# Kernel tuning notes

Hardware: AMD Instinct MI355X
Metric: run time of the kernel (lower is better)

The kernel has to match this reference:

```python
import jax, jax.numpy as jnp
import numpy as np
from jax import lax

B, T, F, H = 64, 512, 512, 1024
NUM_LAYERS = 2


def setup_inputs() -> dict:
    key = jax.random.key(0)
    ks = jax.random.split(key, 9)
    s = 0.05  # small init scale to keep gates in a sane range
    inp = {
        "x": jax.random.normal(ks[0], (B, T, F), dtype=jnp.float32),
        "W_ih_0": jax.random.normal(ks[1], (4 * H, F), dtype=jnp.float32) * s,
        "W_hh_0": jax.random.normal(ks[2], (4 * H, H), dtype=jnp.float32) * s,
        "b_ih_0": jax.random.normal(ks[3], (4 * H,), dtype=jnp.float32) * s,
        "b_hh_0": jax.random.normal(ks[4], (4 * H,), dtype=jnp.float32) * s,
        "W_ih_1": jax.random.normal(ks[5], (4 * H, H), dtype=jnp.float32) * s,
        "W_hh_1": jax.random.normal(ks[6], (4 * H, H), dtype=jnp.float32) * s,
        "b_ih_1": jax.random.normal(ks[7], (4 * H,), dtype=jnp.float32) * s,
        "b_hh_1": jax.random.normal(ks[8], (4 * H,), dtype=jnp.float32) * s,
    }
    return inp


def _lstm_cell(xin, h, c, Wi, Wh, bi, bh):
    # PyTorch LSTMCell: gates ordered (i, f, g, o)
    gates = xin @ Wi.T + h @ Wh.T + bi + bh  # [B, 4H]
    i, f, g, o = jnp.split(gates, 4, axis=-1)
    c_new = jax.nn.sigmoid(f) * c + jax.nn.sigmoid(i) * jnp.tanh(g)
    h_new = jax.nn.sigmoid(o) * jnp.tanh(c_new)
    return h_new, c_new


def reference(x, W_ih_0, W_hh_0, b_ih_0, b_hh_0, W_ih_1, W_hh_1, b_ih_1, b_hh_1):
    params = [(W_ih_0, W_hh_0, b_ih_0, b_hh_0), (W_ih_1, W_hh_1, b_ih_1, b_hh_1)]
    bsz = x.shape[0]

    def step(carry, xt):
        hs, cs = carry
        new_h, new_c = [], []
        inp = xt
        for (Wi, Wh, bi, bh), h, c in zip(params, hs, cs):
            h, c = _lstm_cell(inp, h, c, Wi, Wh, bi, bh)
            new_h.append(h)
            new_c.append(c)
            inp = h
        return (tuple(new_h), tuple(new_c)), inp  # top-layer h is the output

    zeros = tuple(jnp.zeros((bsz, H), dtype=x.dtype) for _ in range(NUM_LAYERS))
    (hT, cT), ys = lax.scan(step, (zeros, zeros), jnp.swapaxes(x, 0, 1))  # ys: [T, B, H]
    out = jnp.swapaxes(ys, 0, 1)  # [B, T, H], sequence_channel=1
    # final state: ([num_layers, B, H], [num_layers, B, H]) as in return_full_states=False
    return out, jnp.stack(hT, 0), jnp.stack(cT, 0)
```

## Files before the change

kernel.cpp:

```cpp
#include <hip/hip_runtime.h>

#define TSTEPS 512
#define BATCH  64
#define FEAT   512
#define HID    1024
#define NWG    256
#define NTHR   256

typedef _Float16 half8_t  __attribute__((ext_vector_type(8)));
typedef _Float16 half4_t  __attribute__((ext_vector_type(4)));
typedef float    float4_t __attribute__((ext_vector_type(4)));

__device__ __forceinline__ float sigf(float x)      { return 1.0f / (1.0f + __expf(-x)); }
__device__ __forceinline__ float tanh_fast(float x) { return 2.0f / (1.0f + __expf(-2.0f * x)) - 1.0f; }

__global__ void xpose_kernel(const float* __restrict__ x, _Float16* __restrict__ xT) {
    int idx = blockIdx.x * NTHR + threadIdx.x;
    int f4 = idx & 127;
    int bt = idx >> 7;
    int t = bt & (TSTEPS - 1);
    int b = bt >> 9;
    float4_t v = ((const float4_t*)x)[idx];
    half4_t h;
    h.x = (_Float16)v.x; h.y = (_Float16)v.y; h.z = (_Float16)v.z; h.w = (_Float16)v.w;
    *(half4_t*)(xT + (size_t)(t * BATCH + b) * FEAT + f4 * 4) = h;
}

__device__ __forceinline__ void grid_barrier(unsigned* bar, int line_id, unsigned step) {
    __syncthreads();
    if (threadIdx.x == 0) {
        unsigned* gen  = bar;
        unsigned* root = bar + 32;
        unsigned* line = bar + 64 + 32 * line_id;
        unsigned old = __hip_atomic_fetch_add(line, 1u, __ATOMIC_RELEASE, __HIP_MEMORY_SCOPE_AGENT);
        if (old == 32u * step - 1u) {
            unsigned r = __hip_atomic_fetch_add(root, 1u, __ATOMIC_RELEASE, __HIP_MEMORY_SCOPE_AGENT);
            if (r == 8u * step - 1u)
                __hip_atomic_store(gen, step, __ATOMIC_RELEASE, __HIP_MEMORY_SCOPE_AGENT);
        }
        while (__hip_atomic_load(gen, __ATOMIC_RELAXED, __HIP_MEMORY_SCOPE_AGENT) < step)
            __builtin_amdgcn_s_sleep(1);
    }
    __syncthreads();
    __builtin_amdgcn_fence(__ATOMIC_ACQUIRE, "agent");
}

__global__ __launch_bounds__(NTHR, 1) void lstm_persistent(
    const float* __restrict__ Wih0, const float* __restrict__ Whh0,
    const float* __restrict__ bih0, const float* __restrict__ bhh0,
    const float* __restrict__ Wih1, const float* __restrict__ Whh1,
    const float* __restrict__ bih1, const float* __restrict__ bhh1,
    const _Float16* __restrict__ xT,
    _Float16* __restrict__ h0buf,
    _Float16* __restrict__ h1buf,
    unsigned* __restrict__ bar,
    float* __restrict__ out)
{
    extern __shared__ __align__(16) char smem[];
    _Float16* w0x = (_Float16*)smem;
    _Float16* w0h = w0x + 16 * FEAT;
    _Float16* w1  = w0h + 16 * HID;

    const int wg  = blockIdx.x;
    const int u0  = ((wg & 7) * 32 + (wg >> 3)) * 4;
    const int tid = threadIdx.x;

    for (int idx = tid; idx < 16 * FEAT; idx += NTHR) {
        int m = idx >> 9, k = idx & (FEAT - 1);
        int grow = (m & 3) * HID + u0 + (m >> 2);
        w0x[(((k >> 3) * 16) + m) * 8 + (k & 7)] = (_Float16)Wih0[grow * FEAT + k];
    }
    for (int idx = tid; idx < 16 * HID; idx += NTHR) {
        int m = idx >> 10, k = idx & (HID - 1);
        int grow = (m & 3) * HID + u0 + (m >> 2);
        w0h[(((k >> 3) * 16) + m) * 8 + (k & 7)] = (_Float16)Whh0[grow * HID + k];
    }
    for (int idx = tid; idx < 16 * 2048; idx += NTHR) {
        int m = idx >> 11, k = idx & 2047;
        int grow = (m & 3) * HID + u0 + (m >> 2);
        float v = (k < HID) ? Wih1[grow * HID + k] : Whh1[grow * HID + (k - HID)];
        w1[(((k >> 3) * 16) + m) * 8 + (k & 7)] = (_Float16)v;
    }

    const int lane  = tid & 63;
    const int wv    = tid >> 6;
    const int q     = lane >> 4;
    const int n     = lane & 15;
    const int batch = wv * 16 + n;
    const int unit  = u0 + q;

    float b0r[4], b1r[4];
#pragma unroll
    for (int r = 0; r < 4; ++r) {
        int grow = r * HID + unit;
        b0r[r] = bih0[grow] + bhh0[grow];
        b1r[r] = bih1[grow] + bhh1[grow];
    }

    __syncthreads();

    const half8_t* a0x = (const half8_t*)w0x;
    const half8_t* a0h = (const half8_t*)w0h;
    const half8_t* a1  = (const half8_t*)w1;
    const float4_t fzero = {0.f, 0.f, 0.f, 0.f};

    float c0 = 0.f, c1 = 0.f, h0v = 0.f, h1v = 0.f;
    float4_t acc[4];
    half8_t  xreg[16];

    {
        const _Float16* xb = xT + (size_t)batch * FEAT + q * 8;
        acc[0] = fzero; acc[1] = fzero; acc[2] = fzero; acc[3] = fzero;
#pragma unroll
        for (int s = 0; s < 16; ++s)
            acc[s & 3] = __builtin_amdgcn_mfma_f32_16x16x32_f16(
                a0x[(s * 4 + q) * 16 + n], *(const half8_t*)(xb + s * 32), acc[s & 3], 0, 0, 0);
        float4_t g = (acc[0] + acc[1]) + (acc[2] + acc[3]);
        float I = sigf(g.x + b0r[0]);
        float G = tanh_fast(g.z + b0r[2]);
        float O = sigf(g.w + b0r[3]);
        c0  = I * G;
        h0v = O * tanh_fast(c0);
        h0buf[batch * HID + unit] = (_Float16)h0v;
    }
    {
        const _Float16* xb = xT + ((size_t)BATCH + batch) * FEAT + q * 8;
#pragma unroll
        for (int s = 0; s < 16; ++s) xreg[s] = *(const half8_t*)(xb + s * 32);
    }
    grid_barrier(bar, wg & 7, 1u);

    for (int t = 0; t < TSTEPS; ++t) {
        const _Float16* h0cur = h0buf + (t & 1) * (BATCH * HID) + batch * HID + q * 8;
        half8_t p0r[32];
#pragma unroll
        for (int s = 0; s < 32; ++s) p0r[s] = *(const half8_t*)(h0cur + s * 32);

        acc[0] = fzero; acc[1] = fzero; acc[2] = fzero; acc[3] = fzero;
#pragma unroll 8
        for (int s = 0; s < 32; ++s)
            acc[s & 3] = __builtin_amdgcn_mfma_f32_16x16x32_f16(
                a1[(s * 4 + q) * 16 + n], p0r[s], acc[s & 3], 0, 0, 0);
        {
            const _Float16* p1 = h1buf + ((t & 1) ^ 1) * (BATCH * HID) + batch * HID + q * 8;
#pragma unroll 8
            for (int s = 0; s < 32; ++s)
                acc[s & 3] = __builtin_amdgcn_mfma_f32_16x16x32_f16(
                    a1[(128 + s * 4 + q) * 16 + n], *(const half8_t*)(p1 + s * 32), acc[s & 3], 0, 0, 0);
        }
        {
            float4_t g = (acc[0] + acc[1]) + (acc[2] + acc[3]);
            float I = sigf(g.x + b1r[0]);
            float F = sigf(g.y + b1r[1]);
            float G = tanh_fast(g.z + b1r[2]);
            float O = sigf(g.w + b1r[3]);
            c1  = F * c1 + I * G;
            h1v = O * tanh_fast(c1);
        }
        h1buf[(t & 1) * (BATCH * HID) + batch * HID + unit] = (_Float16)h1v;
        out[((size_t)batch * TSTEPS + t) * HID + unit] = h1v;

        if (t + 1 < TSTEPS) {
            if (t + 2 < TSTEPS) {
                const _Float16* xb = xT + ((size_t)(t + 2) * BATCH + batch) * FEAT + q * 8;
#pragma unroll
                for (int s = 0; s < 16; ++s) xreg[s] = *(const half8_t*)(xb + s * 32);
            }
            acc[0] = fzero; acc[1] = fzero; acc[2] = fzero; acc[3] = fzero;
#pragma unroll 8
            for (int s = 0; s < 16; ++s)
                acc[s & 3] = __builtin_amdgcn_mfma_f32_16x16x32_f16(
                    a0x[(s * 4 + q) * 16 + n], xreg[s], acc[s & 3], 0, 0, 0);
#pragma unroll 8
            for (int s = 0; s < 32; ++s)
                acc[s & 3] = __builtin_amdgcn_mfma_f32_16x16x32_f16(
                    a0h[(s * 4 + q) * 16 + n], p0r[s], acc[s & 3], 0, 0, 0);
            {
                float4_t g = (acc[0] + acc[1]) + (acc[2] + acc[3]);
                float I = sigf(g.x + b0r[0]);
                float F = sigf(g.y + b0r[1]);
                float G = tanh_fast(g.z + b0r[2]);
                float O = sigf(g.w + b0r[3]);
                c0  = F * c0 + I * G;
                h0v = O * tanh_fast(c0);
            }
            h0buf[((t + 1) & 1) * (BATCH * HID) + batch * HID + unit] = (_Float16)h0v;
            grid_barrier(bar, wg & 7, (unsigned)(t + 2));
        }
    }

    float* hT = out + (size_t)BATCH * TSTEPS * HID;
    float* cT = hT + 2 * BATCH * HID;
    hT[batch * HID + unit]               = h0v;
    hT[BATCH * HID + batch * HID + unit] = h1v;
    cT[batch * HID + unit]               = c0;
    cT[BATCH * HID + batch * HID + unit] = c1;
}

__global__ __launch_bounds__(NTHR, 1) void lstm_persistent2(
    const float* __restrict__ Wih0, const float* __restrict__ Whh0,
    const float* __restrict__ bih0, const float* __restrict__ bhh0,
    const float* __restrict__ Wih1, const float* __restrict__ Whh1,
    const float* __restrict__ bih1, const float* __restrict__ bhh1,
    const _Float16* __restrict__ xT,
    _Float16* __restrict__ h0buf, _Float16* __restrict__ h1buf,
    unsigned* __restrict__ bar, float* __restrict__ out)
{
    extern __shared__ __align__(16) char smem[];
    _Float16* w0x = (_Float16*)smem;
    _Float16* w0h = w0x + 16 * FEAT;
    _Float16* w1  = w0h + 16 * HID;

    const int wg  = blockIdx.x;
    const int u0  = ((wg & 7) * 32 + (wg >> 3)) * 4;
    const int tid = threadIdx.x;

    for (int idx = tid; idx < 16 * FEAT; idx += NTHR) {
        int m = idx >> 9, k = idx & (FEAT - 1);
        int grow = (m & 3) * HID + u0 + (m >> 2);
        w0x[(((k >> 3) * 16) + m) * 8 + (k & 7)] = (_Float16)Wih0[grow * FEAT + k];
    }
    for (int idx = tid; idx < 16 * HID; idx += NTHR) {
        int m = idx >> 10, k = idx & (HID - 1);
        int grow = (m & 3) * HID + u0 + (m >> 2);
        w0h[(((k >> 3) * 16) + m) * 8 + (k & 7)] = (_Float16)Whh0[grow * HID + k];
    }
    for (int idx = tid; idx < 16 * 2048; idx += NTHR) {
        int m = idx >> 11, k = idx & 2047;
        int grow = (m & 3) * HID + u0 + (m >> 2);
        float v = (k < HID) ? Wih1[grow * HID + k] : Whh1[grow * HID + (k - HID)];
        w1[(((k >> 3) * 16) + m) * 8 + (k & 7)] = (_Float16)v;
    }

    const int lane  = tid & 63;
    const int wv    = tid >> 6;
    const int q     = lane >> 4;
    const int n     = lane & 15;
    const int batch = wv * 16 + n;
    const int unit  = u0 + q;

    float b0r[4], b1r[4];
#pragma unroll
    for (int r = 0; r < 4; ++r) {
        int grow = r * HID + unit;
        b0r[r] = bih0[grow] + bhh0[grow];
        b1r[r] = bih1[grow] + bhh1[grow];
    }

    __syncthreads();

    const half8_t* a0x = (const half8_t*)w0x;
    const half8_t* a0h = (const half8_t*)w0h;
    const half8_t* a1  = (const half8_t*)w1;
    const float4_t fzero = {0.f, 0.f, 0.f, 0.f};

    float c0 = 0.f, c1 = 0.f, h0v = 0.f, h1v = 0.f;
    float4_t acc[4];
    half8_t  xreg[16];

    {
        const _Float16* xb = xT + (size_t)batch * FEAT + q * 8;
        acc[0] = fzero; acc[1] = fzero; acc[2] = fzero; acc[3] = fzero;
#pragma unroll
        for (int s = 0; s < 16; ++s)
            acc[s & 3] = __builtin_amdgcn_mfma_f32_16x16x32_f16(
                a0x[(s * 4 + q) * 16 + n], *(const half8_t*)(xb + s * 32), acc[s & 3], 0, 0, 0);
        float4_t g = (acc[0] + acc[1]) + (acc[2] + acc[3]);
        float I = sigf(g.x + b0r[0]);
        float G = tanh_fast(g.z + b0r[2]);
        float O = sigf(g.w + b0r[3]);
        c0  = I * G;
        h0v = O * tanh_fast(c0);
        h0buf[batch * HID + unit] = (_Float16)h0v;
    }
    {
        const _Float16* xb = xT + ((size_t)BATCH + batch) * FEAT + q * 8;
#pragma unroll
        for (int s = 0; s < 16; ++s) xreg[s] = *(const half8_t*)(xb + s * 32);
    }
    grid_barrier(bar, wg & 7, 1u);

    for (int t = 0; t < TSTEPS; ++t) {
        const _Float16* h0cur = h0buf + (t & 1) * (BATCH * HID) + batch * HID + q * 8;
        half8_t p0r[32];
#pragma unroll
        for (int s = 0; s < 32; ++s) p0r[s] = *(const half8_t*)(h0cur + s * 32);

        acc[0] = fzero; acc[1] = fzero; acc[2] = fzero; acc[3] = fzero;
#pragma unroll 8
        for (int s = 0; s < 32; ++s)
            acc[s & 3] = __builtin_amdgcn_mfma_f32_16x16x32_f16(
                a1[(s * 4 + q) * 16 + n], p0r[s], acc[s & 3], 0, 0, 0);
        {
            const _Float16* p1 = h1buf + ((t & 1) ^ 1) * (BATCH * HID) + batch * HID + q * 8;
#pragma unroll 8
            for (int s = 0; s < 32; ++s)
                acc[s & 3] = __builtin_amdgcn_mfma_f32_16x16x32_f16(
                    a1[(128 + s * 4 + q) * 16 + n], *(const half8_t*)(p1 + s * 32), acc[s & 3], 0, 0, 0);
        }
        {
            float4_t g = (acc[0] + acc[1]) + (acc[2] + acc[3]);
            float I = sigf(g.x + b1r[0]);
            float F = sigf(g.y + b1r[1]);
            float G = tanh_fast(g.z + b1r[2]);
            float O = sigf(g.w + b1r[3]);
            c1  = F * c1 + I * G;
            h1v = O * tanh_fast(c1);
        }
        h1buf[(t & 1) * (BATCH * HID) + batch * HID + unit] = (_Float16)h1v;
        out[((size_t)batch * TSTEPS + t) * HID + unit] = h1v;

        if (t + 1 < TSTEPS) {
            acc[0] = fzero; acc[1] = fzero; acc[2] = fzero; acc[3] = fzero;
#pragma unroll 8
            for (int s = 0; s < 16; ++s)
                acc[s & 3] = __builtin_amdgcn_mfma_f32_16x16x32_f16(
                    a0x[(s * 4 + q) * 16 + n], xreg[s], acc[s & 3], 0, 0, 0);
#pragma unroll 8
            for (int s = 0; s < 32; ++s)
                acc[s & 3] = __builtin_amdgcn_mfma_f32_16x16x32_f16(
                    a0h[(s * 4 + q) * 16 + n], p0r[s], acc[s & 3], 0, 0, 0);
            {
                float4_t g = (acc[0] + acc[1]) + (acc[2] + acc[3]);
                float I = sigf(g.x + b0r[0]);
                float F = sigf(g.y + b0r[1]);
                float G = tanh_fast(g.z + b0r[2]);
                float O = sigf(g.w + b0r[3]);
                c0  = F * c0 + I * G;
                h0v = O * tanh_fast(c0);
            }
            h0buf[((t + 1) & 1) * (BATCH * HID) + batch * HID + unit] = (_Float16)h0v;
            if (t + 2 < TSTEPS) {
                const _Float16* xb = xT + ((size_t)(t + 2) * BATCH + batch) * FEAT + q * 8;
#pragma unroll
                for (int s = 0; s < 16; ++s) xreg[s] = *(const half8_t*)(xb + s * 32);
            }
            grid_barrier(bar, wg & 7, (unsigned)(t + 2));
        }
    }

    float* hT = out + (size_t)BATCH * TSTEPS * HID;
    float* cT = hT + 2 * BATCH * HID;
    hT[batch * HID + unit]               = h0v;
    hT[BATCH * HID + batch * HID + unit] = h1v;
    cT[batch * HID + unit]               = c0;
    cT[BATCH * HID + batch * HID + unit] = c1;
}

extern "C" void kernel_launch(void* const* d_in, const int* in_sizes, int n_in,
                              void* d_out, int out_size, void* d_ws, size_t ws_size,
                              hipStream_t stream) {
    (void)in_sizes; (void)n_in; (void)out_size; (void)ws_size;
    const float* x    = (const float*)d_in[0];
    const float* Wih0 = (const float*)d_in[1];
    const float* Whh0 = (const float*)d_in[2];
    const float* bih0 = (const float*)d_in[3];
    const float* bhh0 = (const float*)d_in[4];
    const float* Wih1 = (const float*)d_in[5];
    const float* Whh1 = (const float*)d_in[6];
    const float* bih1 = (const float*)d_in[7];
    const float* bhh1 = (const float*)d_in[8];

    char* ws = (char*)d_ws;
    unsigned* bar   = (unsigned*)ws;
    _Float16* h0buf = (_Float16*)(ws + 4096);
    _Float16* h1buf = (_Float16*)(ws + 4096 + 2 * BATCH * HID * sizeof(_Float16));
    _Float16* xT    = (_Float16*)(ws + (1 << 20));

    hipMemsetAsync(d_ws, 0, 1 << 20, stream);

    xpose_kernel<<<(BATCH * TSTEPS * FEAT / 4) / NTHR, NTHR, 0, stream>>>(x, xT);

    const int shmem = 16 * (FEAT + HID + 2048) * (int)sizeof(_Float16);
    hipFuncSetAttribute((const void*)lstm_persistent2,
                        hipFuncAttributeMaxDynamicSharedMemorySize, shmem);
    lstm_persistent2<<<NWG, NTHR, shmem, stream>>>(
        Wih0, Whh0, bih0, bhh0, Wih1, Whh1, bih1, bhh1,
        xT, h0buf, h1buf, bar, (float*)d_out);
}
```

Measured before the change: 22.06 ms.

## Stage hidden states per XCD with crew copy and drop transpose kernel

Each workgroup detects its XCD, and the workgroups on an XCD cooperatively copy the global h0/h1 state and the fp16-converted next x slice into a per-XCD staging buffer after each grid barrier. A second per-XCD barrier then lets compute read from the XCD-local copy, so it hits that XCD's L2 instead of cross-XCD lines. The separate x transpose kernel is removed and the x conversion is folded into the crew copy. This adds an extra barrier and a copy phase on the critical path of every timestep.

Result: slower. 26.75 ms (+21.2%).

```diff
diff --git a/kernel.cpp b/kernel.cpp
--- a/kernel.cpp
+++ b/kernel.cpp
@@ -6,25 +6,17 @@
 #define HID    1024
 #define NWG    256
 #define NTHR   256
-
+#define WPL    (BATCH * HID / 4)
+#define STGULL 40960
+#define AGENT  __HIP_MEMORY_SCOPE_AGENT
+
+typedef unsigned long long ull;
 typedef _Float16 half8_t  __attribute__((ext_vector_type(8)));
 typedef _Float16 half4_t  __attribute__((ext_vector_type(4)));
 typedef float    float4_t __attribute__((ext_vector_type(4)));
 
 __device__ __forceinline__ float sigf(float x)      { return 1.0f / (1.0f + __expf(-x)); }
 __device__ __forceinline__ float tanh_fast(float x) { return 2.0f / (1.0f + __expf(-2.0f * x)) - 1.0f; }
-
-__global__ void xpose_kernel(const float* __restrict__ x, _Float16* __restrict__ xT) {
-    int idx = blockIdx.x * NTHR + threadIdx.x;
-    int f4 = idx & 127;
-    int bt = idx >> 7;
-    int t = bt & (TSTEPS - 1);
-    int b = bt >> 9;
-    float4_t v = ((const float4_t*)x)[idx];
-    half4_t h;
-    h.x = (_Float16)v.x; h.y = (_Float16)v.y; h.z = (_Float16)v.z; h.w = (_Float16)v.w;
-    *(half4_t*)(xT + (size_t)(t * BATCH + b) * FEAT + f4 * 4) = h;
-}
 
 __device__ __forceinline__ void grid_barrier(unsigned* bar, int line_id, unsigned step) {
     __syncthreads();
@@ -32,27 +24,74 @@
         unsigned* gen  = bar;
         unsigned* root = bar + 32;
         unsigned* line = bar + 64 + 32 * line_id;
-        unsigned old = __hip_atomic_fetch_add(line, 1u, __ATOMIC_RELEASE, __HIP_MEMORY_SCOPE_AGENT);
+        unsigned old = __hip_atomic_fetch_add(line, 1u, __ATOMIC_RELEASE, AGENT);
         if (old == 32u * step - 1u) {
-            unsigned r = __hip_atomic_fetch_add(root, 1u, __ATOMIC_RELEASE, __HIP_MEMORY_SCOPE_AGENT);
+            unsigned r = __hip_atomic_fetch_add(root, 1u, __ATOMIC_RELEASE, AGENT);
             if (r == 8u * step - 1u)
-                __hip_atomic_store(gen, step, __ATOMIC_RELEASE, __HIP_MEMORY_SCOPE_AGENT);
-        }
-        while (__hip_atomic_load(gen, __ATOMIC_RELAXED, __HIP_MEMORY_SCOPE_AGENT) < step)
+                __hip_atomic_store(gen, step, __ATOMIC_RELEASE, AGENT);
+        }
+        while (__hip_atomic_load(gen, __ATOMIC_RELAXED, AGENT) < step)
             __builtin_amdgcn_s_sleep(1);
     }
     __syncthreads();
     __builtin_amdgcn_fence(__ATOMIC_ACQUIRE, "agent");
 }
 
-__global__ __launch_bounds__(NTHR, 1) void lstm_persistent(
+__device__ __forceinline__ void xbar_sync(unsigned* xb, int tid, unsigned target) {
+    __syncthreads();
+    if (tid == 0) {
+        __hip_atomic_fetch_add(xb, 1u, __ATOMIC_RELEASE, AGENT);
+        while (__hip_atomic_load(xb, __ATOMIC_RELAXED, AGENT) < target)
+            __builtin_amdgcn_s_sleep(1);
+    }
+    __syncthreads();
+    asm volatile("" ::: "memory");
+    __builtin_amdgcn_sched_barrier(0);
+}
+
+__device__ __forceinline__ void crew_copy(ull* stg, const ull* h0src, const ull* h1src,
+                                          const float* x, int t2, int do_x,
+                                          int slot, int tid, int crewN) {
+    if (crewN == 32) {
+        int idx = slot * NTHR + tid;
+        ull a = h0src[idx];
+        ull b = h0src[idx + 8192];
+        ull c = h1src[idx];
+        ull d = h1src[idx + 8192];
+        stg[idx]         = a;  stg[idx + 8192]         = b;
+        stg[16384 + idx] = c;  stg[16384 + idx + 8192] = d;
+        if (do_x) {
+            int bb = idx >> 7, f4 = idx & 127;
+            float4_t v = *(const float4_t*)(x + ((size_t)bb * TSTEPS + t2) * FEAT + f4 * 4);
+            half4_t h;
+            h.x = (_Float16)v.x; h.y = (_Float16)v.y; h.z = (_Float16)v.z; h.w = (_Float16)v.w;
+            ((half4_t*)(stg + 32768))[idx] = h;
+        }
+    } else {
+        for (int w = slot * NTHR + tid; w < 16384; w += crewN * NTHR) {
+            stg[w]         = h0src[w];
+            stg[16384 + w] = h1src[w];
+        }
+        if (do_x)
+            for (int idx = slot * NTHR + tid; idx < 8192; idx += crewN * NTHR) {
+                int bb = idx >> 7, f4 = idx & 127;
+                float4_t v = *(const float4_t*)(x + ((size_t)bb * TSTEPS + t2) * FEAT + f4 * 4);
+                half4_t h;
+                h.x = (_Float16)v.x; h.y = (_Float16)v.y; h.z = (_Float16)v.z; h.w = (_Float16)v.w;
+                ((half4_t*)(stg + 32768))[idx] = h;
+            }
+    }
+}
+
+__global__ __launch_bounds__(NTHR, 1) void lstm_persistent4(
     const float* __restrict__ Wih0, const float* __restrict__ Whh0,
     const float* __restrict__ bih0, const float* __restrict__ bhh0,
     const float* __restrict__ Wih1, const float* __restrict__ Whh1,
     const float* __restrict__ bih1, const float* __restrict__ bhh1,
-    const _Float16* __restrict__ xT,
-    _Float16* __restrict__ h0buf,
-    _Float16* __restrict__ h1buf,
+    const float* __restrict__ xf,
+    ull* __restrict__ hx0,
+    ull* __restrict__ hx1,
+    ull* __restrict__ stage,
     unsigned* __restrict__ bar,
     float* __restrict__ out)
 {
@@ -60,10 +99,21 @@
     _Float16* w0x = (_Float16*)smem;
     _Float16* w0h = w0x + 16 * FEAT;
     _Float16* w1  = w0h + 16 * HID;
+    int* comm = (int*)(w1 + 16 * 2048);
 
     const int wg  = blockIdx.x;
     const int u0  = ((wg & 7) * 32 + (wg >> 3)) * 4;
     const int tid = threadIdx.x;
+
+    unsigned* crewcnt = bar + 512;
+    unsigned* xbars   = bar + 1024;
+
+    if (tid == 0) {
+        unsigned xcc = __builtin_amdgcn_s_getreg(63508) & 15u;
+        unsigned slot = __hip_atomic_fetch_add(crewcnt + 32 * xcc, 1u, __ATOMIC_RELAXED, AGENT);
+        comm[0] = (int)xcc;
+        comm[1] = (int)slot;
+    }
 
     for (int idx = tid; idx < 16 * FEAT; idx += NTHR) {
         int m = idx >> 9, k = idx & (FEAT - 1);
@@ -99,6 +149,18 @@
 
     __syncthreads();
 
+    const int xcd  = comm[0];
+    const int slot = comm[1];
+    unsigned* xbar = xbars + 32 * xcd;
+    ull* stg       = stage + (size_t)xcd * STGULL;
+    const _Float16* sh   = (const _Float16*)stg;
+    const _Float16* myh0 = sh + batch * HID + q * 8;
+    const _Float16* myh1 = sh + BATCH * HID + batch * HID + q * 8;
+    const _Float16* myx  = sh + 2 * BATCH * HID + batch * FEAT + q * 8;
+
+    _Float16* hx0h = (_Float16*)hx0;
+    _Float16* hx1h = (_Float16*)hx1;
+
     const half8_t* a0x = (const half8_t*)w0x;
     const half8_t* a0h = (const half8_t*)w0h;
     const half8_t* a1  = (const half8_t*)w1;
@@ -106,48 +168,52 @@
 
     float c0 = 0.f, c1 = 0.f, h0v = 0.f, h1v = 0.f;
     float4_t acc[4];
-    half8_t  xreg[16];
 
     {
-        const _Float16* xb = xT + (size_t)batch * FEAT + q * 8;
+        const float* xb = xf + (size_t)batch * (TSTEPS * FEAT) + q * 8;
         acc[0] = fzero; acc[1] = fzero; acc[2] = fzero; acc[3] = fzero;
 #pragma unroll
-        for (int s = 0; s < 16; ++s)
+        for (int s = 0; s < 16; ++s) {
+            float4_t v0 = *(const float4_t*)(xb + s * 32);
+            float4_t v1 = *(const float4_t*)(xb + s * 32 + 4);
+            half8_t xfr;
+            xfr[0] = (_Float16)v0.x; xfr[1] = (_Float16)v0.y;
+            xfr[2] = (_Float16)v0.z; xfr[3] = (_Float16)v0.w;
+            xfr[4] = (_Float16)v1.x; xfr[5] = (_Float16)v1.y;
+            xfr[6] = (_Float16)v1.z; xfr[7] = (_Float16)v1.w;
             acc[s & 3] = __builtin_amdgcn_mfma_f32_16x16x32_f16(
-                a0x[(s * 4 + q) * 16 + n], *(const half8_t*)(xb + s * 32), acc[s & 3], 0, 0, 0);
+                a0x[(s * 4 + q) * 16 + n], xfr, acc[s & 3], 0, 0, 0);
+        }
         float4_t g = (acc[0] + acc[1]) + (acc[2] + acc[3]);
         float I = sigf(g.x + b0r[0]);
         float G = tanh_fast(g.z + b0r[2]);
         float O = sigf(g.w + b0r[3]);
         c0  = I * G;
         h0v = O * tanh_fast(c0);
-        h0buf[batch * HID + unit] = (_Float16)h0v;
-    }
-    {
-        const _Float16* xb = xT + ((size_t)BATCH + batch) * FEAT + q * 8;
-#pragma unroll
-        for (int s = 0; s < 16; ++s) xreg[s] = *(const half8_t*)(xb + s * 32);
+        hx0h[batch * HID + unit] = (_Float16)h0v;
     }
     grid_barrier(bar, wg & 7, 1u);
+    if (tid == 0)
+        comm[2] = (int)__hip_atomic_load(crewcnt + 32 * xcd, __ATOMIC_RELAXED, AGENT);
+    __syncthreads();
+    const int crewN = comm[2];
+    crew_copy(stg, hx0, hx1 + WPL, xf, 1, 1, slot, tid, crewN);
+    xbar_sync(xbar, tid, (unsigned)crewN);
 
     for (int t = 0; t < TSTEPS; ++t) {
-        const _Float16* h0cur = h0buf + (t & 1) * (BATCH * HID) + batch * HID + q * 8;
         half8_t p0r[32];
 #pragma unroll
-        for (int s = 0; s < 32; ++s) p0r[s] = *(const half8_t*)(h0cur + s * 32);
+        for (int s = 0; s < 32; ++s) p0r[s] = *(const half8_t*)(myh0 + s * 32);
 
         acc[0] = fzero; acc[1] = fzero; acc[2] = fzero; acc[3] = fzero;
 #pragma unroll 8
         for (int s = 0; s < 32; ++s)
             acc[s & 3] = __builtin_amdgcn_mfma_f32_16x16x32_f16(
                 a1[(s * 4 + q) * 16 + n], p0r[s], acc[s & 3], 0, 0, 0);
-        {
-            const _Float16* p1 = h1buf + ((t & 1) ^ 1) * (BATCH * HID) + batch * HID + q * 8;
-#pragma unroll 8
-            for (int s = 0; s < 32; ++s)
-                acc[s & 3] = __builtin_amdgcn_mfma_f32_16x16x32_f16(
-                    a1[(128 + s * 4 + q) * 16 + n], *(const half8_t*)(p1 + s * 32), acc[s & 3], 0, 0, 0);
-        }
+#pragma unroll 8
+        for (int s = 0; s < 32; ++s)
+            acc[s & 3] = __builtin_amdgcn_mfma_f32_16x16x32_f16(
+                a1[(128 + s * 4 + q) * 16 + n], *(const half8_t*)(myh1 + s * 32), acc[s & 3], 0, 0, 0);
         {
             float4_t g = (acc[0] + acc[1]) + (acc[2] + acc[3]);
             float I = sigf(g.x + b1r[0]);
@@ -157,20 +223,16 @@
             c1  = F * c1 + I * G;
             h1v = O * tanh_fast(c1);
         }
-        h1buf[(t & 1) * (BATCH * HID) + batch * HID + unit] = (_Float16)h1v;
         out[((size_t)batch * TSTEPS + t) * HID + unit] = h1v;
 
         if (t + 1 < TSTEPS) {
-            if (t + 2 < TSTEPS) {
-                const _Float16* xb = xT + ((size_t)(t + 2) * BATCH + batch) * FEAT + q * 8;
-#pragma unroll
-                for (int s = 0; s < 16; ++s) xreg[s] = *(const half8_t*)(xb + s * 32);
-            }
+            hx1h[(t & 1) * (BATCH * HID) + batch * HID + unit] = (_Float16)h1v;
+
             acc[0] = fzero; acc[1] = fzero; acc[2] = fzero; acc[3] = fzero;
 #pragma unroll 8
             for (int s = 0; s < 16; ++s)
                 acc[s & 3] = __builtin_amdgcn_mfma_f32_16x16x32_f16(
-                    a0x[(s * 4 + q) * 16 + n], xreg[s], acc[s & 3], 0, 0, 0);
+                    a0x[(s * 4 + q) * 16 + n], *(const half8_t*)(myx + s * 32), acc[s & 3], 0, 0, 0);
 #pragma unroll 8
             for (int s = 0; s < 32; ++s)
                 acc[s & 3] = __builtin_amdgcn_mfma_f32_16x16x32_f16(
@@ -184,158 +246,15 @@
                 c0  = F * c0 + I * G;
                 h0v = O * tanh_fast(c0);
             }
-            h0buf[((t + 1) & 1) * (BATCH * HID) + batch * HID + unit] = (_Float16)h0v;
+            hx0h[((t + 1) & 1) * (BATCH * HID) + batch * HID + unit] = (_Float16)h0v;
+
             grid_barrier(bar, wg & 7, (unsigned)(t + 2));
-        }
-    }
-
-    float* hT = out + (size_t)BATCH * TSTEPS * HID;
-    float* cT = hT + 2 * BATCH * HID;
-    hT[batch * HID + unit]               = h0v;
-    hT[BATCH * HID + batch * HID + unit] = h1v;
-    cT[batch * HID + unit]               = c0;
-    cT[BATCH * HID + batch * HID + unit] = c1;
-}
-
-__global__ __launch_bounds__(NTHR, 1) void lstm_persistent2(
-    const float* __restrict__ Wih0, const float* __restrict__ Whh0,
-    const float* __restrict__ bih0, const float* __restrict__ bhh0,
-    const float* __restrict__ Wih1, const float* __restrict__ Whh1,
-    const float* __restrict__ bih1, const float* __restrict__ bhh1,
-    const _Float16* __restrict__ xT,
-    _Float16* __restrict__ h0buf, _Float16* __restrict__ h1buf,
-    unsigned* __restrict__ bar, float* __restrict__ out)
-{
-    extern __shared__ __align__(16) char smem[];
-    _Float16* w0x = (_Float16*)smem;
-    _Float16* w0h = w0x + 16 * FEAT;
-    _Float16* w1  = w0h + 16 * HID;
-
-    const int wg  = blockIdx.x;
-    const int u0  = ((wg & 7) * 32 + (wg >> 3)) * 4;
-    const int tid = threadIdx.x;
-
-    for (int idx = tid; idx < 16 * FEAT; idx += NTHR) {
-        int m = idx >> 9, k = idx & (FEAT - 1);
-        int grow = (m & 3) * HID + u0 + (m >> 2);
-        w0x[(((k >> 3) * 16) + m) * 8 + (k & 7)] = (_Float16)Wih0[grow * FEAT + k];
-    }
-    for (int idx = tid; idx < 16 * HID; idx += NTHR) {
-        int m = idx >> 10, k = idx & (HID - 1);
-        int grow = (m & 3) * HID + u0 + (m >> 2);
-        w0h[(((k >> 3) * 16) + m) * 8 + (k & 7)] = (_Float16)Whh0[grow * HID + k];
-    }
-    for (int idx = tid; idx < 16 * 2048; idx += NTHR) {
-        int m = idx >> 11, k = idx & 2047;
-        int grow = (m & 3) * HID + u0 + (m >> 2);
-        float v = (k < HID) ? Wih1[grow * HID + k] : Whh1[grow * HID + (k - HID)];
-        w1[(((k >> 3) * 16) + m) * 8 + (k & 7)] = (_Float16)v;
-    }
-
-    const int lane  = tid & 63;
-    const int wv    = tid >> 6;
-    const int q     = lane >> 4;
-    const int n     = lane & 15;
-    const int batch = wv * 16 + n;
-    const int unit  = u0 + q;
-
-    float b0r[4], b1r[4];
-#pragma unroll
-    for (int r = 0; r < 4; ++r) {
-        int grow = r * HID + unit;
-        b0r[r] = bih0[grow] + bhh0[grow];
-        b1r[r] = bih1[grow] + bhh1[grow];
-    }
-
-    __syncthreads();
-
-    const half8_t* a0x = (const half8_t*)w0x;
-    const half8_t* a0h = (const half8_t*)w0h;
-    const half8_t* a1  = (const half8_t*)w1;
-    const float4_t fzero = {0.f, 0.f, 0.f, 0.f};
-
-    float c0 = 0.f, c1 = 0.f, h0v = 0.f, h1v = 0.f;
-    float4_t acc[4];
-    half8_t  xreg[16];
-
-    {
-        const _Float16* xb = xT + (size_t)batch * FEAT + q * 8;
-        acc[0] = fzero; acc[1] = fzero; acc[2] = fzero; acc[3] = fzero;
-#pragma unroll
-        for (int s = 0; s < 16; ++s)
-            acc[s & 3] = __builtin_amdgcn_mfma_f32_16x16x32_f16(
-                a0x[(s * 4 + q) * 16 + n], *(const half8_t*)(xb + s * 32), acc[s & 3], 0, 0, 0);
-        float4_t g = (acc[0] + acc[1]) + (acc[2] + acc[3]);
-        float I = sigf(g.x + b0r[0]);
-        float G = tanh_fast(g.z + b0r[2]);
-        float O = sigf(g.w + b0r[3]);
-        c0  = I * G;
-        h0v = O * tanh_fast(c0);
-        h0buf[batch * HID + unit] = (_Float16)h0v;
-    }
-    {
-        const _Float16* xb = xT + ((size_t)BATCH + batch) * FEAT + q * 8;
-#pragma unroll
-        for (int s = 0; s < 16; ++s) xreg[s] = *(const half8_t*)(xb + s * 32);
-    }
-    grid_barrier(bar, wg & 7, 1u);
-
-    for (int t = 0; t < TSTEPS; ++t) {
-        const _Float16* h0cur = h0buf + (t & 1) * (BATCH * HID) + batch * HID + q * 8;
-        half8_t p0r[32];
-#pragma unroll
-        for (int s = 0; s < 32; ++s) p0r[s] = *(const half8_t*)(h0cur + s * 32);
-
-        acc[0] = fzero; acc[1] = fzero; acc[2] = fzero; acc[3] = fzero;
-#pragma unroll 8
-        for (int s = 0; s < 32; ++s)
-            acc[s & 3] = __builtin_amdgcn_mfma_f32_16x16x32_f16(
-                a1[(s * 4 + q) * 16 + n], p0r[s], acc[s & 3], 0, 0, 0);
-        {
-            const _Float16* p1 = h1buf + ((t & 1) ^ 1) * (BATCH * HID) + batch * HID + q * 8;
-#pragma unroll 8
-            for (int s = 0; s < 32; ++s)
-                acc[s & 3] = __builtin_amdgcn_mfma_f32_16x16x32_f16(
-                    a1[(128 + s * 4 + q) * 16 + n], *(const half8_t*)(p1 + s * 32), acc[s & 3], 0, 0, 0);
-        }
-        {
-            float4_t g = (acc[0] + acc[1]) + (acc[2] + acc[3]);
-            float I = sigf(g.x + b1r[0]);
-            float F = sigf(g.y + b1r[1]);
-            float G = tanh_fast(g.z + b1r[2]);
-            float O = sigf(g.w + b1r[3]);
-            c1  = F * c1 + I * G;
-            h1v = O * tanh_fast(c1);
-        }
-        h1buf[(t & 1) * (BATCH * HID) + batch * HID + unit] = (_Float16)h1v;
-        out[((size_t)batch * TSTEPS + t) * HID + unit] = h1v;
-
-        if (t + 1 < TSTEPS) {
-            acc[0] = fzero; acc[1] = fzero; acc[2] = fzero; acc[3] = fzero;
-#pragma unroll 8
-            for (int s = 0; s < 16; ++s)
-                acc[s & 3] = __builtin_amdgcn_mfma_f32_16x16x32_f16(
-                    a0x[(s * 4 + q) * 16 + n], xreg[s], acc[s & 3], 0, 0, 0);
-#pragma unroll 8
-            for (int s = 0; s < 32; ++s)
-                acc[s & 3] = __builtin_amdgcn_mfma_f32_16x16x32_f16(
-                    a0h[(s * 4 + q) * 16 + n], p0r[s], acc[s & 3], 0, 0, 0);
-            {
-                float4_t g = (acc[0] + acc[1]) + (acc[2] + acc[3]);
-                float I = sigf(g.x + b0r[0]);
-                float F = sigf(g.y + b0r[1]);
-                float G = tanh_fast(g.z + b0r[2]);
-                float O = sigf(g.w + b0r[3]);
-                c0  = F * c0 + I * G;
-                h0v = O * tanh_fast(c0);
-            }
-            h0buf[((t + 1) & 1) * (BATCH * HID) + batch * HID + unit] = (_Float16)h0v;
-            if (t + 2 < TSTEPS) {
-                const _Float16* xb = xT + ((size_t)(t + 2) * BATCH + batch) * FEAT + q * 8;
-#pragma unroll
-                for (int s = 0; s < 16; ++s) xreg[s] = *(const half8_t*)(xb + s * 32);
-            }
-            grid_barrier(bar, wg & 7, (unsigned)(t + 2));
+            crew_copy(stg,
+                      hx0 + (size_t)((t + 1) & 1) * WPL,
+                      hx1 + (size_t)(t & 1) * WPL,
+                      xf, t + 2, (t + 2 < TSTEPS) ? 1 : 0,
+                      slot, tid, crewN);
+            xbar_sync(xbar, tid, (unsigned)crewN * (unsigned)(t + 2));
         }
     }
 
@@ -362,19 +281,16 @@
     const float* bhh1 = (const float*)d_in[8];
 
     char* ws = (char*)d_ws;
-    unsigned* bar   = (unsigned*)ws;
-    _Float16* h0buf = (_Float16*)(ws + 4096);
-    _Float16* h1buf = (_Float16*)(ws + 4096 + 2 * BATCH * HID * sizeof(_Float16));
-    _Float16* xT    = (_Float16*)(ws + (1 << 20));
-
+    unsigned* bar = (unsigned*)ws;
+    ull* hx0      = (ull*)(ws + (64 << 10));
+    ull* hx1      = (ull*)(ws + (64 << 10) + (256 << 10));
+    ull* stage    = (ull*)(ws + (1 << 20));
     hipMemsetAsync(d_ws, 0, 1 << 20, stream);
 
-    xpose_kernel<<<(BATCH * TSTEPS * FEAT / 4) / NTHR, NTHR, 0, stream>>>(x, xT);
-
-    const int shmem = 16 * (FEAT + HID + 2048) * (int)sizeof(_Float16);
-    hipFuncSetAttribute((const void*)lstm_persistent2,
+    const int shmem = 16 * (FEAT + HID + 2048) * (int)sizeof(_Float16) + 256;
+    hipFuncSetAttribute((const void*)lstm_persistent4,
                         hipFuncAttributeMaxDynamicSharedMemorySize, shmem);
-    lstm_persistent2<<<NWG, NTHR, shmem, stream>>>(
+    lstm_persistent4<<<NWG, NTHR, shmem, stream>>>(
         Wih0, Whh0, bih0, bhh0, Wih1, Whh1, bih1, bhh1,
-        xT, h0buf, h1buf, bar, (float*)d_out);
-}
+        x, hx0, hx1, stage, bar, (float*)d_out);
+}
```
